# Performance work log

Measured on AMD Instinct MI355X. Metric: run time of the kernel, lower is better.

Reference implementation:

```python
import jax, jax.numpy as jnp
import numpy as np

B, D, C = 4096, 256, 10
KERNEL_MUL = 2.0
KERNEL_NUM = 5


def setup_inputs() -> dict:
    key = jax.random.key(0)
    k1, k2, k3, k4 = jax.random.split(key, 4)
    source = jax.random.normal(k1, (B, D), dtype=jnp.float32)
    target = jax.random.normal(k2, (B, D), dtype=jnp.float32)
    # source_label is consumed as a one-hot matrix by the module
    src_ids = jax.random.randint(k3, (B,), 0, C)
    source_label = jax.nn.one_hot(src_ids, C, dtype=jnp.float32)
    target_logits = jax.random.uniform(k4, (B, C), dtype=jnp.float32)
    return {"source": source, "target": target,
            "source_label": source_label, "target_logits": target_logits}


def _gaussian_kernel(x, y, kernel_mul, kernel_num):
    total = jnp.concatenate([x, y], axis=0)          # [n, d]
    n = total.shape[0]
    sq = jnp.sum(total * total, axis=1)               # [n]
    # ||a-b||^2 = ||a||^2 + ||b||^2 - 2 a.b  (same math, no [n,n,d] tensor)
    l2 = jnp.maximum(sq[:, None] + sq[None, :] - 2.0 * (total @ total.T), 0.0)
    n_f = jnp.asarray(n, l2.dtype)
    bandwidth = jnp.sum(l2) / (n_f * n_f - n_f)
    bandwidth = bandwidth / (kernel_mul ** (kernel_num // 2))
    kernels = jnp.zeros_like(l2)
    for i in range(kernel_num):
        kernels = kernels + jnp.exp(-l2 / (bandwidth * (kernel_mul ** i)))
    return kernels


def _cal_weight(source_label, target_logits, num_class):
    # normalize source one-hot per class column
    s_sum = jnp.sum(source_label, axis=0, keepdims=True)
    s_sum = jnp.where(s_sum == 0, 100.0, s_sum)
    s = source_label / s_sum                           # [Bs, C]
    # hard target labels for presence mask
    t_label = jnp.argmax(target_logits, axis=1)
    t_onehot = jax.nn.one_hot(t_label, num_class, dtype=target_logits.dtype)
    # normalize soft target logits per class column
    t_sum = jnp.sum(target_logits, axis=0, keepdims=True)
    t_sum = jnp.where(t_sum == 0, 100.0, t_sum)
    t = target_logits / t_sum                          # [Bt, C]
    # class is counted only if present in both domains
    mask = (jnp.sum(s, axis=0) > 0) & (jnp.sum(t_onehot, axis=0) > 0)  # [C]
    maskf = mask.astype(s.dtype)
    sm = s * maskf[None, :]
    tm = t * maskf[None, :]
    count = jnp.sum(maskf)
    weight_ss = sm @ sm.T
    weight_tt = tm @ tm.T
    weight_st = sm @ tm.T
    safe = jnp.where(count > 0, count, 1.0)
    weight_ss = jnp.where(count > 0, weight_ss / safe, 0.0)
    weight_tt = jnp.where(count > 0, weight_tt / safe, 0.0)
    weight_st = jnp.where(count > 0, weight_st / safe, 0.0)
    return weight_ss, weight_tt, weight_st


def reference(source, target, source_label, target_logits):
    num_class = target_logits.shape[1]
    bs = source.shape[0]
    w_ss, w_tt, w_st = _cal_weight(source_label, target_logits, num_class)
    kernels = _gaussian_kernel(source, target, KERNEL_MUL, KERNEL_NUM)
    SS = kernels[:bs, :bs]
    TT = kernels[bs:, bs:]
    ST = kernels[:bs, bs:]
    loss = (jnp.sum(w_ss * SS) + jnp.sum(w_tt * TT)
            - 2.0 * jnp.sum(w_st * ST))
    # eval mode: lambda schedule multiplier = 1.0
    return loss * 1.0
```

## Files before the change

kernel.cpp:

```cpp
#include <hip/hip_runtime.h>
#include <hip/hip_bf16.h>

#define N_TOTAL 8192
#define BROWS   4096
#define DDIM    256
#define NCLS    10
#define NB      64
#define NTRI    (NB*(NB+1)/2)
#define K_STEPS 8

typedef __attribute__((ext_vector_type(8))) short bf16x8;
typedef __attribute__((ext_vector_type(4))) float f32x4;
typedef __attribute__((ext_vector_type(2))) float f32x2;

static constexpr size_t OFF_X    = 0;
static constexpr size_t OFF_SQ   = 0x400000;
static constexpr size_t OFF_XU   = 0x408000;
static constexpr size_t OFF_CP   = 0x488000;
static constexpr size_t OFF_CLS  = 0x498000;
static constexpr size_t OFF_PRES = 0x499000;
static constexpr size_t OFF_SC   = 0x49A000;
static constexpr size_t OFF_PART = 0x49B000;


__device__ __forceinline__ void gload_lds16(const void* g, void* l) {
    __builtin_amdgcn_global_load_lds((const __attribute__((address_space(1))) void*)g,
                                     (__attribute__((address_space(3))) void*)l, 16, 0, 0);
}
__device__ __forceinline__ float rne_bf16_val(float x) {
    unsigned b = __float_as_uint(x);
    unsigned r = (b + 0x7FFFu + ((b >> 16) & 1u)) >> 16;
    return __uint_as_float(r << 16);
}

__global__ void k_pre(const float* __restrict__ src, const float* __restrict__ tgt,
                      const float* __restrict__ label, const float* __restrict__ logits,
                      unsigned short* __restrict__ X, float* __restrict__ sq,
                      float* __restrict__ colpart, float* __restrict__ clspart,
                      unsigned* __restrict__ prespart) {
    __shared__ float shbuf[8][256];
    __shared__ float cbuf[256][NCLS];
    __shared__ unsigned pm[128];
    int t = threadIdx.x;
    int bid = blockIdx.x;

    if (bid < 2048) {
        int wid  = t >> 6;
        int lane = t & 63;
        int row  = bid * 4 + wid;
        const float* p = (row < BROWS) ? (src + (size_t)row * DDIM)
                                       : (tgt + (size_t)(row - BROWS) * DDIM);
        f32x4 v = *reinterpret_cast<const f32x4*>(p + lane * 4);
        unsigned short h[4];
        float ssum = 0.f;
#pragma unroll
        for (int e = 0; e < 4; ++e) {
            unsigned bits = __float_as_uint(v[e]);
            unsigned r = (bits + 0x7FFFu + ((bits >> 16) & 1u)) >> 16;
            h[e] = (unsigned short)r;
            float f = __uint_as_float(r << 16);
            ssum += f * f;
        }
        ushort4 us; us.x = h[0]; us.y = h[1]; us.z = h[2]; us.w = h[3];
        *reinterpret_cast<ushort4*>(X + (size_t)row * DDIM + lane * 4) = us;
#pragma unroll
        for (int off = 32; off > 0; off >>= 1) ssum += __shfl_xor(ssum, off);
        if (lane == 0) sq[row] = ssum;
    } else if (bid < 2112) {
        int b  = bid - 2048;
        int cg = t & 31;
        int rs = t >> 5;
        const float* base = (b < 32)
            ? (src + ((size_t)(b * 128 + rs)) * DDIM + cg * 8)
            : (tgt + ((size_t)((b - 32) * 128 + rs)) * DDIM + cg * 8);
        float a[8];
#pragma unroll
        for (int e = 0; e < 8; ++e) a[e] = 0.f;
        for (int i = 0; i < 16; ++i) {
            const float* rp = base + (size_t)i * 8 * DDIM;
            f32x4 v0 = *reinterpret_cast<const f32x4*>(rp);
            f32x4 v1 = *reinterpret_cast<const f32x4*>(rp + 4);
#pragma unroll
            for (int e = 0; e < 4; ++e) a[e]     += rne_bf16_val(v0[e]);
#pragma unroll
            for (int e = 0; e < 4; ++e) a[4 + e] += rne_bf16_val(v1[e]);
        }
#pragma unroll
        for (int e = 0; e < 8; ++e) shbuf[rs][cg * 8 + e] = a[e];
        __syncthreads();
        float s = 0.f;
#pragma unroll
        for (int k = 0; k < 8; ++k) s += shbuf[k][t];
        colpart[b * DDIM + t] = s;
    } else {
        int b = bid - 2112;
        int r = b * 128 + (t & 127);
        if (t < 128) {
            const float* lr = label + (size_t)r * NCLS;
#pragma unroll
            for (int c = 0; c < NCLS; ++c) cbuf[t][c] = lr[c];
        } else {
            const float* gr = logits + (size_t)r * NCLS;
            float bv = -1e30f; int bc = 0;
#pragma unroll
            for (int c = 0; c < NCLS; ++c) {
                float v = gr[c];
                cbuf[t][c] = v;
                if (v > bv) { bv = v; bc = c; }
            }
            pm[t - 128] = 1u << bc;
        }
        __syncthreads();
        if (t < NCLS) {
            float a = 0.f;
            for (int i = 0; i < 128; ++i) a += cbuf[i][t];
            clspart[b * 20 + t] = a;
        } else if (t < 2 * NCLS) {
            float a = 0.f;
            for (int i = 128; i < 256; ++i) a += cbuf[i][t - NCLS];
            clspart[b * 20 + t] = a;
        }
        if (t == 0) {
            unsigned p = 0;
            for (int i = 0; i < 128; ++i) p |= pm[i];
            prespart[b] = p;
        }
    }
}

__global__ void k_scales(const float* __restrict__ clspart, const unsigned* __restrict__ prespart,
                         const float* __restrict__ colpart, const float* __restrict__ sq,
                         const float* __restrict__ label, const float* __restrict__ logits,
                         float* __restrict__ scal, unsigned short* __restrict__ XU) {
    __shared__ float  cfin[2 * NCLS];
    __shared__ float  ascale[NCLS], bscale[NCLS];
    __shared__ unsigned presAll;
    __shared__ double dred[256];
    int t = threadIdx.x, b = blockIdx.x;

    if (t < 2 * NCLS) {
        float a = 0.f;
        for (int k = 0; k < 32; ++k) a += clspart[k * 20 + t];
        cfin[t] = a;
    }
    if (t == 0) {
        unsigned p = 0;
        for (int k = 0; k < 32; ++k) p |= prespart[k];
        presAll = p;
    }
    __syncthreads();
    if (t == 0) {
        int count = 0;
        for (int c = 0; c < NCLS; ++c) {
            float sv = cfin[c], tv = cfin[NCLS + c];
            bool m = (sv > 0.f) && ((presAll >> c) & 1u);
            count += m ? 1 : 0;
            float sdiv = (sv == 0.f) ? 100.f : sv;
            float tdiv = (tv == 0.f) ? 100.f : tv;
            ascale[c] = m ? (1.f / sdiv) : 0.f;
            bscale[c] = m ? (1.f / tdiv) : 0.f;
        }
        if (b == 32) scal[5] = (float)(count > 0 ? count : 1);
    }
    __syncthreads();

    if (b < 32) {
        int r = b * 256 + t;
        float v[NCLS];
        if (r < BROWS) {
            const float* lr = label + (size_t)r * NCLS;
#pragma unroll
            for (int c = 0; c < NCLS; ++c) v[c] = lr[c] * ascale[c];
        } else {
            const float* gr = logits + (size_t)(r - BROWS) * NCLS;
#pragma unroll
            for (int c = 0; c < NCLS; ++c) v[c] = -gr[c] * bscale[c];
        }
        unsigned packed[16];
#pragma unroll
        for (int w = 0; w < 16; ++w) {
            unsigned lo = 0, hi = 0;
            if (2 * w < NCLS) {
                unsigned bits = __float_as_uint(v[2 * w]);
                lo = (bits + 0x7FFFu + ((bits >> 16) & 1u)) >> 16;
            }
            if (2 * w + 1 < NCLS) {
                unsigned bits = __float_as_uint(v[2 * w + 1]);
                hi = (bits + 0x7FFFu + ((bits >> 16) & 1u)) >> 16;
            }
            packed[w] = lo | (hi << 16);
        }
        uint4* out = reinterpret_cast<uint4*>(XU + (size_t)r * 32);
#pragma unroll
        for (int q = 0; q < 4; ++q)
            out[q] = make_uint4(packed[4*q], packed[4*q+1], packed[4*q+2], packed[4*q+3]);
    } else {
        double cd = 0.0;
        for (int k = 0; k < 64; ++k) cd += (double)colpart[k * DDIM + t];
        dred[t] = cd * cd;
        __syncthreads();
        for (int s = 128; s > 0; s >>= 1) { if (t < s) dred[t] += dred[t + s]; __syncthreads(); }
        double S_cs = dred[0];
        __syncthreads();
        double ss = 0.0;
        for (int k = 0; k < 32; ++k) ss += (double)sq[t + 256 * k];
        dred[t] = ss;
        __syncthreads();
        for (int s = 128; s > 0; s >>= 1) { if (t < s) dred[t] += dred[t + s]; __syncthreads(); }
        if (t == 0) {
            double nf = (double)N_TOTAL;
            double sum_l2 = 2.0 * nf * dred[0] - 2.0 * S_cs;
            if (sum_l2 < 0.0) sum_l2 = 0.0;
            double bw = sum_l2 / (nf * nf - nf) / 4.0;
            scal[0] = (float)(-1.0 / (16.0 * bw));
        }
    }
}

__global__ __launch_bounds__(256, 3) void k_main(const unsigned short* __restrict__ X,
                                                 const unsigned short* __restrict__ XU,
                                                 const float* __restrict__ sq,
                                                 const float* __restrict__ scal,
                                                 double* __restrict__ partials) {
    int bid = (blockIdx.x & 7) * (NTRI / 8) + (blockIdx.x >> 3);
    int bi = 0, rem = bid;
    while (rem >= NB - bi) { rem -= NB - bi; ++bi; }
    int bj = bi + rem;

    int tid = threadIdx.x, lane = tid & 63, wid = tid >> 6;
    int wr = wid >> 1, wc = wid & 1;
    int lrow = lane & 15, kgrp = lane >> 4;

    __shared__ unsigned short Abuf[2 * 128 * 32];
    __shared__ unsigned short Bbuf[2 * 128 * 32];
    __shared__ float red[4];
    char* AB = (char*)Abuf;
    char* BB = (char*)Bbuf;

    float nb = scal[0];

    f32x4 acc[4][4];
#pragma unroll
    for (int a = 0; a < 4; ++a)
#pragma unroll
        for (int b = 0; b < 4; ++b) acc[a][b] = (f32x4){0.f, 0.f, 0.f, 0.f};

    const unsigned short* gA0 = X + ((size_t)bi * 128 + (tid >> 2)) * DDIM + (tid & 3) * 8;
    const unsigned short* gA1 = gA0 + (size_t)64 * DDIM;
    const unsigned short* gB0 = X + ((size_t)bj * 128 + (tid >> 2)) * DDIM + (tid & 3) * 8;
    const unsigned short* gB1 = gB0 + (size_t)64 * DDIM;
    int lds0 = tid * 16;
    int aoff = (wr * 64 + lrow) * 64 + kgrp * 16;
    int boff = (wc * 64 + lrow) * 64 + kgrp * 16;

#define STAGE(BS, KS) do { \
    gload_lds16(gA0 + (KS) * 32, AB + (BS) * 8192 + lds0); \
    gload_lds16(gA1 + (KS) * 32, AB + (BS) * 8192 + lds0 + 4096); \
    gload_lds16(gB0 + (KS) * 32, BB + (BS) * 8192 + lds0); \
    gload_lds16(gB1 + (KS) * 32, BB + (BS) * 8192 + lds0 + 4096); \
} while (0)

#define COMPUTE(BS) do { \
    bf16x8 af[4], bf[4]; \
    _Pragma("unroll") \
    for (int f = 0; f < 4; ++f) { \
        af[f] = *reinterpret_cast<const bf16x8*>(AB + (BS) * 8192 + aoff + f * 1024); \
        bf[f] = *reinterpret_cast<const bf16x8*>(BB + (BS) * 8192 + boff + f * 1024); \
    } \
    _Pragma("unroll") \
    for (int a = 0; a < 4; ++a) \
        _Pragma("unroll") \
        for (int b = 0; b < 4; ++b) \
            acc[a][b] = __builtin_amdgcn_mfma_f32_16x16x32_bf16(af[a], bf[b], acc[a][b], 0, 0, 0); \
} while (0)

    STAGE(0, 0);
    __syncthreads();
#pragma unroll
    for (int t = 0; t < K_STEPS - 1; ++t) {
        STAGE((t + 1) & 1, t + 1);
        COMPUTE(t & 1);
        __syncthreads();
    }

    int i0 = bi * 128 + wr * 64;
    int j0 = bj * 128 + wc * 64;
    const unsigned short* AU = XU + (size_t)(i0 + lrow) * 32 + kgrp * 8;
    const unsigned short* BU = XU + (size_t)(j0 + lrow) * 32 + kgrp * 8;
    bf16x8 au[4], bu[4];
#pragma unroll
    for (int f = 0; f < 4; ++f) {
        au[f] = *reinterpret_cast<const bf16x8*>(AU + (size_t)f * 16 * 32);
        bu[f] = *reinterpret_cast<const bf16x8*>(BU + (size_t)f * 16 * 32);
    }
    f32x4 sqin[4];
#pragma unroll
    for (int f = 0; f < 4; ++f)
        sqin[f] = *reinterpret_cast<const f32x4*>(sq + i0 + f * 16 + kgrp * 4);
    float sqjn[4];
#pragma unroll
    for (int g = 0; g < 4; ++g) sqjn[g] = sq[j0 + g * 16 + lrow];

    COMPUTE((K_STEPS - 1) & 1);

#pragma unroll
    for (int f = 0; f < 4; ++f) sqin[f] *= nb;
#pragma unroll
    for (int g = 0; g < 4; ++g) sqjn[g] *= nb;
    float m2nb = -2.f * nb;

    f32x2 lp2 = (f32x2){0.f, 0.f};
#pragma unroll
    for (int g = 0; g < 4; ++g) {
        f32x4 wf[4];
#pragma unroll
        for (int f = 0; f < 4; ++f)
            wf[f] = __builtin_amdgcn_mfma_f32_16x16x32_bf16(au[f], bu[g], (f32x4){0.f,0.f,0.f,0.f}, 0, 0, 0);
#pragma unroll
        for (int f = 0; f < 4; ++f) {
#pragma unroll
            for (int h = 0; h < 2; ++h) {
                f32x2 ssn = (f32x2){ sqin[f][2*h] + sqjn[g], sqin[f][2*h+1] + sqjn[g] };
                f32x2 tt  = (f32x2){ fmaf(acc[f][g][2*h],   m2nb, ssn.x),
                                     fmaf(acc[f][g][2*h+1], m2nb, ssn.y) };
                tt.x = fminf(tt.x, 0.f);
                tt.y = fminf(tt.y, 0.f);
                f32x2 e;
                e.x = __expf(tt.x);
                e.y = __expf(tt.y);
                f32x2 e2 = e * e, e4 = e2 * e2, e8 = e4 * e4, e16 = e8 * e8;
                f32x2 ks = ((e + e2) + (e4 + e8)) + e16;
                lp2.x = fmaf(wf[f][2*h],   ks.x, lp2.x);
                lp2.y = fmaf(wf[f][2*h+1], ks.y, lp2.y);
            }
        }
    }
    float lp = lp2.x + lp2.y;

#pragma unroll
    for (int off = 32; off > 0; off >>= 1) lp += __shfl_xor(lp, off);
    if (lane == 0) red[wid] = lp;
    __syncthreads();
    if (tid == 0)
        partials[bid] = (double)((red[0] + red[1]) + (red[2] + red[3])) * ((bi == bj) ? 1.0 : 2.0);
#undef STAGE
#undef COMPUTE
}

__global__ void k_final(const double* __restrict__ partials, const float* __restrict__ scal,
                        float* __restrict__ out) {
    __shared__ double dred[256];
    int t = threadIdx.x;
    double s = 0.0;
    for (int k = 0; k < 9; ++k) {
        int idx = t + 256 * k;
        if (idx < NTRI) s += partials[idx];
    }
    dred[t] = s;
    __syncthreads();
    for (int st = 128; st > 0; st >>= 1) { if (t < st) dred[t] += dred[t + st]; __syncthreads(); }
    if (t == 0) out[0] = (float)(dred[0] / (double)scal[5]);
}

extern "C" void kernel_launch(void* const* d_in, const int* in_sizes, int n_in,
                              void* d_out, int out_size, void* d_ws, size_t ws_size,
                              hipStream_t stream) {
    const float* src    = (const float*)d_in[0];
    const float* tgt    = (const float*)d_in[1];
    const float* label  = (const float*)d_in[2];
    const float* logits = (const float*)d_in[3];

    char* ws = (char*)d_ws;
    unsigned short* X   = (unsigned short*)(ws + OFF_X);
    float* sq           = (float*)(ws + OFF_SQ);
    unsigned short* XU  = (unsigned short*)(ws + OFF_XU);
    float* colpart      = (float*)(ws + OFF_CP);
    float* clspart      = (float*)(ws + OFF_CLS);
    unsigned* prespart  = (unsigned*)(ws + OFF_PRES);
    float* scal         = (float*)(ws + OFF_SC);
    double* partials    = (double*)(ws + OFF_PART);

    k_pre    <<<2144, 256, 0, stream>>>(src, tgt, label, logits, X, sq, colpart, clspart, prespart);
    k_scales <<<33,   256, 0, stream>>>(clspart, prespart, colpart, sq, label, logits, scal, XU);
    k_main   <<<NTRI, 256, 0, stream>>>(X, XU, sq, scal, partials);
    k_final  <<<1,    256, 0, stream>>>(partials, scal, (float*)d_out);
}
```

Measured before the change: 56.45 us.

## Deepen k_main LDS pipeline with explicit waits and fuse final reduction

Restructures the K loop of the main MFMA kernel to prefetch two stages ahead, using explicit s_waitcnt and s_barrier with sched_barrier fences so LDS reads finish before the buffer is refilled and global loads overlap the MFMAs. It also removes the separate final-reduction launch: each block bumps an atomic counter after writing its partial, and the last block sums all partials and writes the output. This is meant to hide global-load latency and save one kernel launch. The cost is hand-managed wait counts that are fragile, plus a counter reset that relies on k_pre running first.

Result: slower. 89.51 us (+58.6%).

```diff
diff --git a/kernel.cpp b/kernel.cpp
--- a/kernel.cpp
+++ b/kernel.cpp
@@ -7,7 +7,6 @@
 #define NCLS    10
 #define NB      64
 #define NTRI    (NB*(NB+1)/2)
-#define K_STEPS 8
 
 typedef __attribute__((ext_vector_type(8))) short bf16x8;
 typedef __attribute__((ext_vector_type(4))) float f32x4;
@@ -20,6 +19,7 @@
 static constexpr size_t OFF_CLS  = 0x498000;
 static constexpr size_t OFF_PRES = 0x499000;
 static constexpr size_t OFF_SC   = 0x49A000;
+static constexpr size_t OFF_CTR  = 0x49A800;
 static constexpr size_t OFF_PART = 0x49B000;
 
 
@@ -37,12 +37,13 @@
                       const float* __restrict__ label, const float* __restrict__ logits,
                       unsigned short* __restrict__ X, float* __restrict__ sq,
                       float* __restrict__ colpart, float* __restrict__ clspart,
-                      unsigned* __restrict__ prespart) {
+                      unsigned* __restrict__ prespart, unsigned* __restrict__ ctr) {
     __shared__ float shbuf[8][256];
     __shared__ float cbuf[256][NCLS];
     __shared__ unsigned pm[128];
     int t = threadIdx.x;
     int bid = blockIdx.x;
+    if (bid == 0 && t == 0) *ctr = 0u;
 
     if (bid < 2048) {
         int wid  = t >> 6;
@@ -217,11 +218,21 @@
     }
 }
 
+#define VMW(N)  do { asm volatile("s_waitcnt vmcnt(" #N ")" ::: "memory"); \
+                     __builtin_amdgcn_sched_barrier(0); } while (0)
+#define LGW0    do { asm volatile("s_waitcnt lgkmcnt(0)" ::: "memory"); \
+                     __builtin_amdgcn_sched_barrier(0); } while (0)
+#define BARR    do { __builtin_amdgcn_sched_barrier(0); \
+                     asm volatile("s_barrier" ::: "memory"); \
+                     __builtin_amdgcn_sched_barrier(0); } while (0)
+
 __global__ __launch_bounds__(256, 3) void k_main(const unsigned short* __restrict__ X,
                                                  const unsigned short* __restrict__ XU,
                                                  const float* __restrict__ sq,
                                                  const float* __restrict__ scal,
-                                                 double* __restrict__ partials) {
+                                                 double* __restrict__ partials,
+                                                 unsigned* __restrict__ ctr,
+                                                 float* __restrict__ out) {
     int bid = (blockIdx.x & 7) * (NTRI / 8) + (blockIdx.x >> 3);
     int bi = 0, rem = bid;
     while (rem >= NB - bi) { rem -= NB - bi; ++bi; }
@@ -233,11 +244,11 @@
 
     __shared__ unsigned short Abuf[2 * 128 * 32];
     __shared__ unsigned short Bbuf[2 * 128 * 32];
+    __shared__ double dred2[256];
     __shared__ float red[4];
+    __shared__ unsigned lastflag;
     char* AB = (char*)Abuf;
     char* BB = (char*)Bbuf;
-
-    float nb = scal[0];
 
     f32x4 acc[4][4];
 #pragma unroll
@@ -253,6 +264,8 @@
     int aoff = (wr * 64 + lrow) * 64 + kgrp * 16;
     int boff = (wc * 64 + lrow) * 64 + kgrp * 16;
 
+    bf16x8 af[4], bf_[4];
+
 #define STAGE(BS, KS) do { \
     gload_lds16(gA0 + (KS) * 32, AB + (BS) * 8192 + lds0); \
     gload_lds16(gA1 + (KS) * 32, AB + (BS) * 8192 + lds0 + 4096); \
@@ -260,28 +273,36 @@
     gload_lds16(gB1 + (KS) * 32, BB + (BS) * 8192 + lds0 + 4096); \
 } while (0)
 
-#define COMPUTE(BS) do { \
-    bf16x8 af[4], bf[4]; \
+#define DSREAD(BS) do { \
     _Pragma("unroll") \
     for (int f = 0; f < 4; ++f) { \
-        af[f] = *reinterpret_cast<const bf16x8*>(AB + (BS) * 8192 + aoff + f * 1024); \
-        bf[f] = *reinterpret_cast<const bf16x8*>(BB + (BS) * 8192 + boff + f * 1024); \
-    } \
+        af[f]  = *reinterpret_cast<const bf16x8*>(AB + (BS) * 8192 + aoff + f * 1024); \
+        bf_[f] = *reinterpret_cast<const bf16x8*>(BB + (BS) * 8192 + boff + f * 1024); \
+    } } while (0)
+
+#define DOMFMA() do { \
     _Pragma("unroll") \
     for (int a = 0; a < 4; ++a) \
         _Pragma("unroll") \
         for (int b = 0; b < 4; ++b) \
-            acc[a][b] = __builtin_amdgcn_mfma_f32_16x16x32_bf16(af[a], bf[b], acc[a][b], 0, 0, 0); \
-} while (0)
-
-    STAGE(0, 0);
-    __syncthreads();
-#pragma unroll
-    for (int t = 0; t < K_STEPS - 1; ++t) {
-        STAGE((t + 1) & 1, t + 1);
-        COMPUTE(t & 1);
-        __syncthreads();
-    }
+            acc[a][b] = __builtin_amdgcn_mfma_f32_16x16x32_bf16(af[a], bf_[b], acc[a][b], 0, 0, 0); \
+    } while (0)
+
+#define STEP_STAGE(T) do { \
+    DSREAD((T) & 1); LGW0; BARR; \
+    STAGE((T) & 1, (T) + 2); \
+    DOMFMA(); VMW(4); BARR; } while (0)
+
+    STAGE(0, 0); STAGE(1, 1);
+    VMW(4); BARR;
+
+    STEP_STAGE(0); STEP_STAGE(1); STEP_STAGE(2);
+    STEP_STAGE(3); STEP_STAGE(4); STEP_STAGE(5);
+
+    DSREAD(0); LGW0; BARR;
+    DOMFMA(); VMW(0); BARR;
+
+    DSREAD(1); LGW0;
 
     int i0 = bi * 128 + wr * 64;
     int j0 = bj * 128 + wc * 64;
@@ -300,8 +321,9 @@
     float sqjn[4];
 #pragma unroll
     for (int g = 0; g < 4; ++g) sqjn[g] = sq[j0 + g * 16 + lrow];
-
-    COMPUTE((K_STEPS - 1) & 1);
+    float nb = scal[0];
+
+    DOMFMA();
 
 #pragma unroll
     for (int f = 0; f < 4; ++f) sqin[f] *= nb;
@@ -341,25 +363,34 @@
     for (int off = 32; off > 0; off >>= 1) lp += __shfl_xor(lp, off);
     if (lane == 0) red[wid] = lp;
     __syncthreads();
-    if (tid == 0)
+    if (tid == 0) {
         partials[bid] = (double)((red[0] + red[1]) + (red[2] + red[3])) * ((bi == bj) ? 1.0 : 2.0);
+        __threadfence();
+        unsigned old = atomicAdd(ctr, 1u);
+        lastflag = (old == NTRI - 1) ? 1u : 0u;
+    }
+    __syncthreads();
+
+    if (lastflag) {
+        __threadfence();
+        const volatile double* vp = partials;
+        double s = 0.0;
+        for (int k = 0; k < 9; ++k) {
+            int idx = tid + 256 * k;
+            if (idx < NTRI) s += vp[idx];
+        }
+        dred2[tid] = s;
+        __syncthreads();
+        for (int st = 128; st > 0; st >>= 1) {
+            if (tid < st) dred2[tid] += dred2[tid + st];
+            __syncthreads();
+        }
+        if (tid == 0) out[0] = (float)(dred2[0] / (double)scal[5]);
+    }
 #undef STAGE
-#undef COMPUTE
-}
-
-__global__ void k_final(const double* __restrict__ partials, const float* __restrict__ scal,
-                        float* __restrict__ out) {
-    __shared__ double dred[256];
-    int t = threadIdx.x;
-    double s = 0.0;
-    for (int k = 0; k < 9; ++k) {
-        int idx = t + 256 * k;
-        if (idx < NTRI) s += partials[idx];
-    }
-    dred[t] = s;
-    __syncthreads();
-    for (int st = 128; st > 0; st >>= 1) { if (t < st) dred[t] += dred[t + st]; __syncthreads(); }
-    if (t == 0) out[0] = (float)(dred[0] / (double)scal[5]);
+#undef DSREAD
+#undef DOMFMA
+#undef STEP_STAGE
 }
 
 extern "C" void kernel_launch(void* const* d_in, const int* in_sizes, int n_in,
@@ -378,10 +409,10 @@
     float* clspart      = (float*)(ws + OFF_CLS);
     unsigned* prespart  = (unsigned*)(ws + OFF_PRES);
     float* scal         = (float*)(ws + OFF_SC);
+    unsigned* ctr       = (unsigned*)(ws + OFF_CTR);
     double* partials    = (double*)(ws + OFF_PART);
 
-    k_pre    <<<2144, 256, 0, stream>>>(src, tgt, label, logits, X, sq, colpart, clspart, prespart);
+    k_pre    <<<2144, 256, 0, stream>>>(src, tgt, label, logits, X, sq, colpart, clspart, prespart, ctr);
     k_scales <<<33,   256, 0, stream>>>(clspart, prespart, colpart, sq, label, logits, scal, XU);
-    k_main   <<<NTRI, 256, 0, stream>>>(X, XU, sq, scal, partials);
-    k_final  <<<1,    256, 0, stream>>>(partials, scal, (float*)d_out);
-}
+    k_main   <<<NTRI, 256, 0, stream>>>(X, XU, sq, scal, partials, ctr, (float*)d_out);
+}
```
